# Optimization experiments

Measured on AMD Instinct MI355X. Metric: run time of the kernel, lower is better.

## Reference

```python
import jax, jax.numpy as jnp
import numpy as np

NUM_ITERATIONS = 3

def _squash(t, axis=-1):
    # norm here is the SQUARED norm, matching the torch code exactly
    norm = jnp.sum(t * t, axis=axis, keepdims=True)
    scale = norm / (1.0 + norm)
    return scale * t / jnp.sqrt(norm)

def setup_inputs() -> dict:
    key = jax.random.key(0)
    k1, k2 = jax.random.split(key)
    B, R, Cin = 1024, 2336, 4  # batch, num_routes, primary_capslen
    K, Cout = 2, 16            # num_caps, digital_capslen
    u = jax.random.normal(k1, (B, R, Cin), dtype=jnp.float32)
    W = jax.random.normal(k2, (K, R, Cin, Cout), dtype=jnp.float32)
    return {"u": u, "W": W}

def reference(u, W):
    # u: [B,R,Cin]; W: [K,R,Cin,Cout]
    # torch: u[:,None,:,None,:] @ W -> [B,K,R,1,Cout]; we drop the singleton.
    u_ji = jnp.einsum('bri,krio->bkro', u, W)  # [B,K,R,Cout]
    B, K, R, Cout = u_ji.shape
    # b is constant along the Cout axis (zeros init + delta_b keepdim), so keep it [B,K,R,1]
    b = jnp.zeros((B, K, R, 1), dtype=u_ji.dtype)
    v = None
    for i in range(NUM_ITERATIONS):
        c = jax.nn.softmax(b, axis=2)                      # softmax over routes (dim=2)
        s = jnp.sum(c * u_ji, axis=2, keepdims=True)       # [B,K,1,Cout]
        v = _squash(s, axis=-1)                            # [B,K,1,Cout]
        if i != NUM_ITERATIONS - 1:
            delta_b = jnp.sum(u_ji * v, axis=-1, keepdims=True)  # [B,K,R,1]
            b = b + delta_b
    v = jnp.squeeze(v, axis=2)                             # [B,K,Cout]
    classes = jnp.sqrt(jnp.sum(v * v, axis=-1))            # [B,K]
    return jax.nn.softmax(classes, axis=-1)                # F.softmax default dim=1 on 2D
```

## Files before the change

### kernel.cpp

```cpp
#include <hip/hip_runtime.h>
#include <stdint.h>

#define RT    2336
#define RLDS  1952
#define RRES  (RT - RLDS)
#define NTH   512
#define NBLK  2048
#define BATCH 1024
#define SH1   32.0f
#define SH2   64.0f

__device__ __forceinline__ float blo(uint32_t v){ union {uint32_t u; float f;} x; x.u = v << 16;        return x.f; }
__device__ __forceinline__ float bhi(uint32_t v){ union {uint32_t u; float f;} x; x.u = v & 0xffff0000u; return x.f; }
__device__ __forceinline__ uint32_t f2b1(float f){
  union {float f; uint32_t u;} x; x.f = f;
  return (x.u + 0x7fffu + ((x.u >> 16) & 1u)) >> 16;
}
__device__ __forceinline__ uint32_t f2b_pack(float a, float b){ return f2b1(a) | (f2b1(b) << 16); }

__device__ __forceinline__ void merge_quad(float4& a, float l, int tid,
                                           float (*red)[4][5], float* vbuf,
                                           bool last, float* out_cls){
  #pragma unroll
  for (int off = 32; off >= 4; off >>= 1){
    a.x += __shfl_down(a.x, off); a.y += __shfl_down(a.y, off);
    a.z += __shfl_down(a.z, off); a.w += __shfl_down(a.w, off);
    l   += __shfl_down(l,   off);
  }
  const int lane = tid & 63, wid = tid >> 6;
  if (lane < 4){
    red[wid][lane][0] = l;
    red[wid][lane][1] = a.x; red[wid][lane][2] = a.y;
    red[wid][lane][3] = a.z; red[wid][lane][4] = a.w;
  }
  __syncthreads();
  if (tid == 0){
    float L = 0.f, S[16];
    #pragma unroll
    for (int o = 0; o < 16; ++o) S[o] = 0.f;
    for (int w = 0; w < 8; ++w){
      #pragma unroll
      for (int q = 0; q < 4; ++q){
        L += red[w][q][0];
        #pragma unroll
        for (int j = 0; j < 4; ++j) S[4*q+j] += red[w][q][1+j];
      }
    }
    L *= 0.25f;
    float inv = 1.f / L, norm = 0.f;
    #pragma unroll
    for (int o = 0; o < 16; ++o){ S[o] *= inv; norm += S[o]*S[o]; }
    if (last){
      *out_cls = norm / (1.f + norm);
    } else {
      float f = sqrtf(norm) / (1.f + norm);
      #pragma unroll
      for (int o = 0; o < 16; ++o) vbuf[o] = S[o] * f;
    }
  }
  __syncthreads();
}

__global__ void __launch_bounds__(NTH, 4)
caps_route(const float* __restrict__ U, const float* __restrict__ W,
           float* __restrict__ Out){
  __shared__ uint2 uj[RLDS * 4];
  __shared__ float red[8][4][5];
  __shared__ float vbuf[16];

  const int tid = threadIdx.x;
  const int qo  = tid & 3;
  const int k   = blockIdx.x & 1;
  const int b   = blockIdx.x >> 1;

  const float* Ub = U + (size_t)b * (RT * 4);
  const float* Wk = W + (size_t)k * ((size_t)RT * 64) + qo * 4;

  float4 acc; float l;
  float  ur[3][4];
  float  d1[16], d1r[3];
  float  vc0, vc1, vc2, vc3;

  auto build_rq = [&](int route) -> float4 {
    float4 u4 = *(const float4*)(Ub + (size_t)route * 4);
    const float* wr = Wk + (size_t)route * 64;
    float4 w0 = *(const float4*)(wr);
    float4 w1 = *(const float4*)(wr + 16);
    float4 w2 = *(const float4*)(wr + 32);
    float4 w3 = *(const float4*)(wr + 48);
    float4 p;
    p.x = u4.x * w0.x; p.y = u4.x * w0.y; p.z = u4.x * w0.z; p.w = u4.x * w0.w;
    p.x = fmaf(u4.y, w1.x, p.x); p.y = fmaf(u4.y, w1.y, p.y);
    p.z = fmaf(u4.y, w1.z, p.z); p.w = fmaf(u4.y, w1.w, p.w);
    p.x = fmaf(u4.z, w2.x, p.x); p.y = fmaf(u4.z, w2.y, p.y);
    p.z = fmaf(u4.z, w2.z, p.z); p.w = fmaf(u4.z, w2.w, p.w);
    p.x = fmaf(u4.w, w3.x, p.x); p.y = fmaf(u4.w, w3.y, p.y);
    p.z = fmaf(u4.w, w3.z, p.z); p.w = fmaf(u4.w, w3.w, p.w);
    return p;
  };

  acc = make_float4(0.f, 0.f, 0.f, 0.f); l = 0.f;

  if (tid < 128){
    int route = tid >> 2;
    float4 p = build_rq(route);
    acc.x += p.x; acc.y += p.y; acc.z += p.z; acc.w += p.w; l += 1.f;
    uj[route*4 + qo] = make_uint2(f2b_pack(p.x, p.y), f2b_pack(p.z, p.w));
  }
  #pragma unroll 3
  for (int s = 0; s < 18; ++s){
    int route = 32 + s*128 + (tid >> 2);
    float4 p = build_rq(route);
    acc.x += p.x; acc.y += p.y; acc.z += p.z; acc.w += p.w; l += 1.f;
    if (s < 15){
      uj[route*4 + qo] = make_uint2(f2b_pack(p.x, p.y), f2b_pack(p.z, p.w));
    } else {
      int slot = s - 15;
      ur[slot][0] = p.x; ur[slot][1] = p.y; ur[slot][2] = p.z; ur[slot][3] = p.w;
    }
  }
  merge_quad(acc, l, tid, red, vbuf, false, nullptr);
  vc0 = vbuf[4*qo]; vc1 = vbuf[4*qo+1]; vc2 = vbuf[4*qo+2]; vc3 = vbuf[4*qo+3];

  acc = make_float4(0.f, 0.f, 0.f, 0.f); l = 0.f;
  #pragma unroll 4
  for (int s = 0; s < 16; ++s){
    int idx = tid + (s << 9);
    bool act = (idx < RLDS * 4);
    float uf0=0.f, uf1=0.f, uf2=0.f, uf3=0.f, d = 0.f;
    if (act){
      uint2 q2 = uj[idx];
      uf0 = blo(q2.x); uf1 = bhi(q2.x); uf2 = blo(q2.y); uf3 = bhi(q2.y);
      d = fmaf(uf0, vc0, fmaf(uf1, vc1, fmaf(uf2, vc2, uf3 * vc3)));
    }
    d += __shfl_xor(d, 1); d += __shfl_xor(d, 2);
    d1[s] = d;
    if (act){
      float e = __expf(d - SH1);
      l += e;
      acc.x = fmaf(e, uf0, acc.x); acc.y = fmaf(e, uf1, acc.y);
      acc.z = fmaf(e, uf2, acc.z); acc.w = fmaf(e, uf3, acc.w);
    }
  }
  #pragma unroll
  for (int slot = 0; slot < 3; ++slot){
    float d = fmaf(ur[slot][0], vc0, fmaf(ur[slot][1], vc1,
              fmaf(ur[slot][2], vc2, ur[slot][3] * vc3)));
    d += __shfl_xor(d, 1); d += __shfl_xor(d, 2);
    d1r[slot] = d;
    float e = __expf(d - SH1);
    l += e;
    acc.x = fmaf(e, ur[slot][0], acc.x); acc.y = fmaf(e, ur[slot][1], acc.y);
    acc.z = fmaf(e, ur[slot][2], acc.z); acc.w = fmaf(e, ur[slot][3], acc.w);
  }
  merge_quad(acc, l, tid, red, vbuf, false, nullptr);
  vc0 = vbuf[4*qo]; vc1 = vbuf[4*qo+1]; vc2 = vbuf[4*qo+2]; vc3 = vbuf[4*qo+3];

  acc = make_float4(0.f, 0.f, 0.f, 0.f); l = 0.f;
  #pragma unroll 4
  for (int s = 0; s < 16; ++s){
    int idx = tid + (s << 9);
    bool act = (idx < RLDS * 4);
    float uf0=0.f, uf1=0.f, uf2=0.f, uf3=0.f, d = 0.f;
    if (act){
      uint2 q2 = uj[idx];
      uf0 = blo(q2.x); uf1 = bhi(q2.x); uf2 = blo(q2.y); uf3 = bhi(q2.y);
      d = fmaf(uf0, vc0, fmaf(uf1, vc1, fmaf(uf2, vc2, uf3 * vc3)));
    }
    d += __shfl_xor(d, 1); d += __shfl_xor(d, 2);
    d += d1[s];
    if (act){
      float e = __expf(d - SH2);
      l += e;
      acc.x = fmaf(e, uf0, acc.x); acc.y = fmaf(e, uf1, acc.y);
      acc.z = fmaf(e, uf2, acc.z); acc.w = fmaf(e, uf3, acc.w);
    }
  }
  #pragma unroll
  for (int slot = 0; slot < 3; ++slot){
    float d = fmaf(ur[slot][0], vc0, fmaf(ur[slot][1], vc1,
              fmaf(ur[slot][2], vc2, ur[slot][3] * vc3)));
    d += __shfl_xor(d, 1); d += __shfl_xor(d, 2);
    d += d1r[slot];
    float e = __expf(d - SH2);
    l += e;
    acc.x = fmaf(e, ur[slot][0], acc.x); acc.y = fmaf(e, ur[slot][1], acc.y);
    acc.z = fmaf(e, ur[slot][2], acc.z); acc.w = fmaf(e, ur[slot][3], acc.w);
  }
  merge_quad(acc, l, tid, red, vbuf, true, Out + blockIdx.x);
}

__global__ void caps_softmax(float* __restrict__ Out){
  int b = blockIdx.x * blockDim.x + threadIdx.x;
  if (b < BATCH){
    float2* p = (float2*)Out;
    float2 c = p[b];
    float m  = fmaxf(c.x, c.y);
    float e0 = __expf(c.x - m), e1 = __expf(c.y - m);
    float inv = 1.f / (e0 + e1);
    p[b] = make_float2(e0 * inv, e1 * inv);
  }
}

extern "C" void kernel_launch(void* const* d_in, const int* in_sizes, int n_in,
                              void* d_out, int out_size, void* d_ws, size_t ws_size,
                              hipStream_t stream) {
  const float* U = (const float*)d_in[0];
  const float* W = (const float*)d_in[1];
  float* Out = (float*)d_out;
  caps_route<<<dim3(NBLK), dim3(NTH), 0, stream>>>(U, W, Out);
  caps_softmax<<<dim3(BATCH / 256), dim3(256), 0, stream>>>(Out);
}
```

Baseline: 152.0 us.

## Keep all u_hat values in fp32 registers instead of bf16 shared memory

Each thread now keeps its 19 route predictions as float4 registers (76 VGPRs) instead of packing most of them to bf16 in a 62 KB LDS buffer. The third routing pass reuses the linearity of the logits, taking the dot with v0+v1 rather than storing the first-pass logits. The block reduction in merge_quad is spread across 32 threads with shuffles instead of one serial thread. This removes LDS traffic, bf16 conversion and the LDS occupancy limit, at the cost of heavy register pressure under launch_bounds(512,4).

```diff
diff --git a/kernel.cpp b/kernel.cpp
--- a/kernel.cpp
+++ b/kernel.cpp
@@ -2,23 +2,14 @@
 #include <stdint.h>
 
 #define RT    2336
-#define RLDS  1952
-#define RRES  (RT - RLDS)
 #define NTH   512
+#define NSL   19
 #define NBLK  2048
 #define BATCH 1024
 #define SH1   32.0f
 #define SH2   64.0f
 
-__device__ __forceinline__ float blo(uint32_t v){ union {uint32_t u; float f;} x; x.u = v << 16;        return x.f; }
-__device__ __forceinline__ float bhi(uint32_t v){ union {uint32_t u; float f;} x; x.u = v & 0xffff0000u; return x.f; }
-__device__ __forceinline__ uint32_t f2b1(float f){
-  union {float f; uint32_t u;} x; x.f = f;
-  return (x.u + 0x7fffu + ((x.u >> 16) & 1u)) >> 16;
-}
-__device__ __forceinline__ uint32_t f2b_pack(float a, float b){ return f2b1(a) | (f2b1(b) << 16); }
-
-__device__ __forceinline__ void merge_quad(float4& a, float l, int tid,
+__device__ __forceinline__ void merge_quad(float4 a, float l, int tid,
                                            float (*red)[4][5], float* vbuf,
                                            bool last, float* out_cls){
   #pragma unroll
@@ -34,28 +25,29 @@
     red[wid][lane][3] = a.z; red[wid][lane][4] = a.w;
   }
   __syncthreads();
-  if (tid == 0){
-    float L = 0.f, S[16];
+  if (tid < 32){
+    int w = tid >> 2, q = tid & 3;
+    float L  = red[w][q][0];
+    float s0 = red[w][q][1], s1 = red[w][q][2];
+    float s2 = red[w][q][3], s3 = red[w][q][4];
     #pragma unroll
-    for (int o = 0; o < 16; ++o) S[o] = 0.f;
-    for (int w = 0; w < 8; ++w){
-      #pragma unroll
-      for (int q = 0; q < 4; ++q){
-        L += red[w][q][0];
-        #pragma unroll
-        for (int j = 0; j < 4; ++j) S[4*q+j] += red[w][q][1+j];
+    for (int off = 16; off >= 4; off >>= 1){
+      L  += __shfl_down(L,  off);
+      s0 += __shfl_down(s0, off); s1 += __shfl_down(s1, off);
+      s2 += __shfl_down(s2, off); s3 += __shfl_down(s3, off);
+    }
+    float inv = 1.f / L;
+    s0 *= inv; s1 *= inv; s2 *= inv; s3 *= inv;
+    float nq = s0*s0 + s1*s1 + s2*s2 + s3*s3;
+    nq += __shfl_xor(nq, 1); nq += __shfl_xor(nq, 2);
+    if (tid < 4){
+      if (last){
+        if (tid == 0) *out_cls = nq / (1.f + nq);
+      } else {
+        float f = sqrtf(nq) / (1.f + nq);
+        vbuf[4*tid+0] = s0*f; vbuf[4*tid+1] = s1*f;
+        vbuf[4*tid+2] = s2*f; vbuf[4*tid+3] = s3*f;
       }
-    }
-    L *= 0.25f;
-    float inv = 1.f / L, norm = 0.f;
-    #pragma unroll
-    for (int o = 0; o < 16; ++o){ S[o] *= inv; norm += S[o]*S[o]; }
-    if (last){
-      *out_cls = norm / (1.f + norm);
-    } else {
-      float f = sqrtf(norm) / (1.f + norm);
-      #pragma unroll
-      for (int o = 0; o < 16; ++o) vbuf[o] = S[o] * f;
     }
   }
   __syncthreads();
@@ -64,128 +56,79 @@
 __global__ void __launch_bounds__(NTH, 4)
 caps_route(const float* __restrict__ U, const float* __restrict__ W,
            float* __restrict__ Out){
-  __shared__ uint2 uj[RLDS * 4];
   __shared__ float red[8][4][5];
   __shared__ float vbuf[16];
 
   const int tid = threadIdx.x;
   const int qo  = tid & 3;
+  const int rg  = tid >> 2;
   const int k   = blockIdx.x & 1;
   const int b   = blockIdx.x >> 1;
 
   const float* Ub = U + (size_t)b * (RT * 4);
   const float* Wk = W + (size_t)k * ((size_t)RT * 64) + qo * 4;
 
-  float4 acc; float l;
-  float  ur[3][4];
-  float  d1[16], d1r[3];
-  float  vc0, vc1, vc2, vc3;
+  float4 uj[NSL];
+  float4 acc = make_float4(0.f,0.f,0.f,0.f);
+  float  l = 0.f;
 
-  auto build_rq = [&](int route) -> float4 {
-    float4 u4 = *(const float4*)(Ub + (size_t)route * 4);
-    const float* wr = Wk + (size_t)route * 64;
-    float4 w0 = *(const float4*)(wr);
-    float4 w1 = *(const float4*)(wr + 16);
-    float4 w2 = *(const float4*)(wr + 32);
-    float4 w3 = *(const float4*)(wr + 48);
-    float4 p;
-    p.x = u4.x * w0.x; p.y = u4.x * w0.y; p.z = u4.x * w0.z; p.w = u4.x * w0.w;
-    p.x = fmaf(u4.y, w1.x, p.x); p.y = fmaf(u4.y, w1.y, p.y);
-    p.z = fmaf(u4.y, w1.z, p.z); p.w = fmaf(u4.y, w1.w, p.w);
-    p.x = fmaf(u4.z, w2.x, p.x); p.y = fmaf(u4.z, w2.y, p.y);
-    p.z = fmaf(u4.z, w2.z, p.z); p.w = fmaf(u4.z, w2.w, p.w);
-    p.x = fmaf(u4.w, w3.x, p.x); p.y = fmaf(u4.w, w3.y, p.y);
-    p.z = fmaf(u4.w, w3.z, p.z); p.w = fmaf(u4.w, w3.w, p.w);
-    return p;
-  };
-
-  acc = make_float4(0.f, 0.f, 0.f, 0.f); l = 0.f;
-
-  if (tid < 128){
-    int route = tid >> 2;
-    float4 p = build_rq(route);
-    acc.x += p.x; acc.y += p.y; acc.z += p.z; acc.w += p.w; l += 1.f;
-    uj[route*4 + qo] = make_uint2(f2b_pack(p.x, p.y), f2b_pack(p.z, p.w));
-  }
-  #pragma unroll 3
-  for (int s = 0; s < 18; ++s){
-    int route = 32 + s*128 + (tid >> 2);
-    float4 p = build_rq(route);
-    acc.x += p.x; acc.y += p.y; acc.z += p.z; acc.w += p.w; l += 1.f;
-    if (s < 15){
-      uj[route*4 + qo] = make_uint2(f2b_pack(p.x, p.y), f2b_pack(p.z, p.w));
+  #pragma unroll
+  for (int s = 0; s < NSL; ++s){
+    if (s < NSL-1 || tid < 128){
+      int route = s*128 + rg;
+      float4 u4 = *(const float4*)(Ub + (size_t)route * 4);
+      const float* wr = Wk + (size_t)route * 64;
+      float4 w0 = *(const float4*)(wr);
+      float4 w1 = *(const float4*)(wr + 16);
+      float4 w2 = *(const float4*)(wr + 32);
+      float4 w3 = *(const float4*)(wr + 48);
+      float4 p;
+      p.x = u4.x * w0.x; p.y = u4.x * w0.y; p.z = u4.x * w0.z; p.w = u4.x * w0.w;
+      p.x = fmaf(u4.y, w1.x, p.x); p.y = fmaf(u4.y, w1.y, p.y);
+      p.z = fmaf(u4.y, w1.z, p.z); p.w = fmaf(u4.y, w1.w, p.w);
+      p.x = fmaf(u4.z, w2.x, p.x); p.y = fmaf(u4.z, w2.y, p.y);
+      p.z = fmaf(u4.z, w2.z, p.z); p.w = fmaf(u4.z, w2.w, p.w);
+      p.x = fmaf(u4.w, w3.x, p.x); p.y = fmaf(u4.w, w3.y, p.y);
+      p.z = fmaf(u4.w, w3.z, p.z); p.w = fmaf(u4.w, w3.w, p.w);
+      uj[s] = p;
+      acc.x += p.x; acc.y += p.y; acc.z += p.z; acc.w += p.w;
+      l += 1.f;
     } else {
-      int slot = s - 15;
-      ur[slot][0] = p.x; ur[slot][1] = p.y; ur[slot][2] = p.z; ur[slot][3] = p.w;
+      uj[s] = make_float4(0.f,0.f,0.f,0.f);
     }
   }
   merge_quad(acc, l, tid, red, vbuf, false, nullptr);
-  vc0 = vbuf[4*qo]; vc1 = vbuf[4*qo+1]; vc2 = vbuf[4*qo+2]; vc3 = vbuf[4*qo+3];
+  float4 v0 = make_float4(vbuf[4*qo], vbuf[4*qo+1], vbuf[4*qo+2], vbuf[4*qo+3]);
 
-  acc = make_float4(0.f, 0.f, 0.f, 0.f); l = 0.f;
-  #pragma unroll 4
-  for (int s = 0; s < 16; ++s){
-    int idx = tid + (s << 9);
-    bool act = (idx < RLDS * 4);
-    float uf0=0.f, uf1=0.f, uf2=0.f, uf3=0.f, d = 0.f;
-    if (act){
-      uint2 q2 = uj[idx];
-      uf0 = blo(q2.x); uf1 = bhi(q2.x); uf2 = blo(q2.y); uf3 = bhi(q2.y);
-      d = fmaf(uf0, vc0, fmaf(uf1, vc1, fmaf(uf2, vc2, uf3 * vc3)));
-    }
+  acc = make_float4(0.f,0.f,0.f,0.f); l = 0.f;
+  #pragma unroll
+  for (int s = 0; s < NSL; ++s){
+    float4 p = uj[s];
+    float d = fmaf(p.x, v0.x, fmaf(p.y, v0.y, fmaf(p.z, v0.z, p.w * v0.w)));
     d += __shfl_xor(d, 1); d += __shfl_xor(d, 2);
-    d1[s] = d;
-    if (act){
+    if (s < NSL-1 || tid < 128){
       float e = __expf(d - SH1);
       l += e;
-      acc.x = fmaf(e, uf0, acc.x); acc.y = fmaf(e, uf1, acc.y);
-      acc.z = fmaf(e, uf2, acc.z); acc.w = fmaf(e, uf3, acc.w);
+      acc.x = fmaf(e, p.x, acc.x); acc.y = fmaf(e, p.y, acc.y);
+      acc.z = fmaf(e, p.z, acc.z); acc.w = fmaf(e, p.w, acc.w);
     }
   }
+  merge_quad(acc, l, tid, red, vbuf, false, nullptr);
+  float4 vs = make_float4(v0.x + vbuf[4*qo],   v0.y + vbuf[4*qo+1],
+                          v0.z + vbuf[4*qo+2], v0.w + vbuf[4*qo+3]);
+
+  acc = make_float4(0.f,0.f,0.f,0.f); l = 0.f;
   #pragma unroll
-  for (int slot = 0; slot < 3; ++slot){
-    float d = fmaf(ur[slot][0], vc0, fmaf(ur[slot][1], vc1,
-              fmaf(ur[slot][2], vc2, ur[slot][3] * vc3)));
+  for (int s = 0; s < NSL; ++s){
+    float4 p = uj[s];
+    float d = fmaf(p.x, vs.x, fmaf(p.y, vs.y, fmaf(p.z, vs.z, p.w * vs.w)));
     d += __shfl_xor(d, 1); d += __shfl_xor(d, 2);
-    d1r[slot] = d;
-    float e = __expf(d - SH1);
-    l += e;
-    acc.x = fmaf(e, ur[slot][0], acc.x); acc.y = fmaf(e, ur[slot][1], acc.y);
-    acc.z = fmaf(e, ur[slot][2], acc.z); acc.w = fmaf(e, ur[slot][3], acc.w);
-  }
-  merge_quad(acc, l, tid, red, vbuf, false, nullptr);
-  vc0 = vbuf[4*qo]; vc1 = vbuf[4*qo+1]; vc2 = vbuf[4*qo+2]; vc3 = vbuf[4*qo+3];
-
-  acc = make_float4(0.f, 0.f, 0.f, 0.f); l = 0.f;
-  #pragma unroll 4
-  for (int s = 0; s < 16; ++s){
-    int idx = tid + (s << 9);
-    bool act = (idx < RLDS * 4);
-    float uf0=0.f, uf1=0.f, uf2=0.f, uf3=0.f, d = 0.f;
-    if (act){
-      uint2 q2 = uj[idx];
-      uf0 = blo(q2.x); uf1 = bhi(q2.x); uf2 = blo(q2.y); uf3 = bhi(q2.y);
-      d = fmaf(uf0, vc0, fmaf(uf1, vc1, fmaf(uf2, vc2, uf3 * vc3)));
-    }
-    d += __shfl_xor(d, 1); d += __shfl_xor(d, 2);
-    d += d1[s];
-    if (act){
+    if (s < NSL-1 || tid < 128){
       float e = __expf(d - SH2);
       l += e;
-      acc.x = fmaf(e, uf0, acc.x); acc.y = fmaf(e, uf1, acc.y);
-      acc.z = fmaf(e, uf2, acc.z); acc.w = fmaf(e, uf3, acc.w);
+      acc.x = fmaf(e, p.x, acc.x); acc.y = fmaf(e, p.y, acc.y);
+      acc.z = fmaf(e, p.z, acc.z); acc.w = fmaf(e, p.w, acc.w);
     }
-  }
-  #pragma unroll
-  for (int slot = 0; slot < 3; ++slot){
-    float d = fmaf(ur[slot][0], vc0, fmaf(ur[slot][1], vc1,
-              fmaf(ur[slot][2], vc2, ur[slot][3] * vc3)));
-    d += __shfl_xor(d, 1); d += __shfl_xor(d, 2);
-    d += d1r[slot];
-    float e = __expf(d - SH2);
-    l += e;
-    acc.x = fmaf(e, ur[slot][0], acc.x); acc.y = fmaf(e, ur[slot][1], acc.y);
-    acc.z = fmaf(e, ur[slot][2], acc.z); acc.w = fmaf(e, ur[slot][3], acc.w);
   }
   merge_quad(acc, l, tid, red, vbuf, true, Out + blockIdx.x);
 }
```

Measured after the change: 171.6 us. +12.9%, slower.
